# Kernel tuning notes

Measured on AMD Instinct MI355X. Metric: run time of the kernel, lower is better.

Reference implementation:

```python
import jax, jax.numpy as jnp
import numpy as np
import math

HEAD_DIM = 128
DEPTH = 12
LAMBDA_INIT = 0.8 - 0.6 * math.exp(-0.3 * DEPTH)
EPS = 1e-5


def setup_inputs() -> dict:
    key = jax.random.key(0)
    ks = jax.random.split(key, 7)
    B, S, H2, D = 2, 2048, 16, HEAD_DIM  # H2 = 2 * num_diff_heads
    q = jax.random.normal(ks[0], (B, S, H2, D), dtype=jnp.float32)
    k = jax.random.normal(ks[1], (B, S, H2, D), dtype=jnp.float32)
    v = jax.random.normal(ks[2], (B, S, H2, D), dtype=jnp.float32)
    lambda_q1 = 0.1 * jax.random.normal(ks[3], (D,), dtype=jnp.float32)
    lambda_k1 = 0.1 * jax.random.normal(ks[4], (D,), dtype=jnp.float32)
    lambda_q2 = 0.1 * jax.random.normal(ks[5], (D,), dtype=jnp.float32)
    lambda_k2 = 0.1 * jax.random.normal(ks[6], (D,), dtype=jnp.float32)
    return {"q": q, "k": k, "v": v, "lambda_q1": lambda_q1, "lambda_k1": lambda_k1,
            "lambda_q2": lambda_q2, "lambda_k2": lambda_k2}


def _attn(qh, kh, v12, scale, causal_bias):
    # qh,kh: [B,S,H,D]; v12: [B,S,H,2D] (concat of v1,v2 -> same softmax shared,
    # identical math to the two separate flash calls attnX1/attnX2 concatenated)
    scores = jnp.einsum('bshd,bthd->bhst', qh, kh) * scale + causal_bias
    p = jax.nn.softmax(scores, axis=-1)
    return jnp.einsum('bhst,bthd->bshd', p, v12)  # [B,S,H,2D]


def reference(q, k, v, lambda_q1, lambda_k1, lambda_q2, lambda_k2):
    B, S, H2, D = q.shape
    H = H2 // 2
    scale = 1.0 / math.sqrt(D)
    # split_heads: '(H two) D' -> pairs of adjacent heads
    def split(x):
        x = x.reshape(B, S, H, 2, D)
        return x[..., 0, :], x[..., 1, :]
    q1, q2 = split(q)
    k1, k2 = split(k)
    v1, v2 = split(v)
    v12 = jnp.concatenate([v1, v2], axis=-1)  # [B,S,H,2D]

    causal_bias = jnp.where(jnp.tril(jnp.ones((S, S), dtype=bool)), 0.0,
                            jnp.float32(-jnp.inf))  # [S,S]

    attn1 = _attn(q1, k1, v12, scale, causal_bias)  # = cat(attn11, attn12)
    attn2 = _attn(q2, k2, v12, scale, causal_bias)  # = cat(attn21, attn22)

    lambda_1 = jnp.exp(jnp.sum(lambda_q1 * lambda_k1))
    lambda_2 = jnp.exp(jnp.sum(lambda_q2 * lambda_k2))
    lambda_full = lambda_1 - lambda_2 + LAMBDA_INIT

    attn = attn1 - lambda_full * attn2  # [B,S,H,2D]
    # RMSNorm over last dim (2D), no affine
    attn = attn * jax.lax.rsqrt(jnp.mean(attn * attn, axis=-1, keepdims=True) + EPS)
    attn = attn * (1.0 - LAMBDA_INIT)
    # '... H (two D) -> ... (H two) D'
    return attn.reshape(B, S, H, 2, D).reshape(B, S, H2, D)
```

## Files before the change

kernel.cpp:

```cpp
#include <hip/hip_runtime.h>
#include <math.h>


#define S_LEN 2048
#define ROWSTR 2048
#define NEG_BIG (-3.0e38f)
#define QSCALE (1.44269504088896f * 0.0883883476483184f)
#define SM_SHIFT 20.0f
#define LAMBDA_INIT 0.783605766532f

typedef __attribute__((ext_vector_type(8))) short short8;
typedef __attribute__((ext_vector_type(4))) float f32x4;

__device__ __forceinline__ short f2bf(float f) {
    unsigned u = __builtin_bit_cast(unsigned, f);
    u += 0x7fffu + ((u >> 16) & 1u);
    return (short)(u >> 16);
}

__device__ __forceinline__ void async16(const short* g, short* l) {
    __builtin_amdgcn_global_load_lds(
        (const __attribute__((address_space(1))) unsigned int*)g,
        (__attribute__((address_space(3))) unsigned int*)l, 16, 0, 0);
}

__global__ __launch_bounds__(256)
void prep_kernel(const float* __restrict__ k, const float* __restrict__ v,
                 short* __restrict__ kws, short* __restrict__ vws) {
    __shared__ short sKL[8192];
    __shared__ short sT[32][260];
    const int tid = threadIdx.x;
    const int bh  = blockIdx.x >> 6;
    const int t   = blockIdx.x & 63;
    const int b   = bh >> 3;
    const int h   = bh & 7;

    {
        const int lh    = tid & 31;
        const int c     = lh >> 1;
        const int half  = lh & 1;
        const int rbase = tid >> 5;
        #pragma unroll
        for (int p = 0; p < 8; ++p) {
            const int row  = p * 8 + rbase;
            const int attn = row >> 5;
            const int key  = row & 31;
            const float* src = k + (((size_t)(b * S_LEN + t * 32 + key) * 16) + 2 * h + attn) * 128 + lh * 4;
            const float4 a = *(const float4*)src;
            short4 sv;
            sv.x = f2bf(a.x); sv.y = f2bf(a.y); sv.z = f2bf(a.z); sv.w = f2bf(a.w);
            *(short4*)(sKL + attn * 4096 + key * 128 + ((c ^ (key & 7)) << 3) + half * 4) = sv;
        }
    }

    {
        const int n0 = (tid & 63) * 4;
        const int kb = tid >> 6;
        #pragma unroll
        for (int p = 0; p < 8; ++p) {
            const int key = p * 4 + kb;
            const float* src = v + (((size_t)(b * S_LEN + t * 32 + key) * 16) + 2 * h) * 128 + n0;
            const float4 a = *(const float4*)src;
            short4 sv;
            sv.x = f2bf(a.x); sv.y = f2bf(a.y); sv.z = f2bf(a.z); sv.w = f2bf(a.w);
            *(short4*)(&sT[key][n0]) = sv;
        }
    }
    __syncthreads();

    {
        short* kdst = kws + (((size_t)(bh * 64 + t)) << 13);
        #pragma unroll
        for (int i = 0; i < 4; ++i) {
            const short8 d = *(const short8*)(sKL + i * 2048 + tid * 8);
            *(short8*)(kdst + i * 2048 + tid * 8) = d;
        }
    }

    {
        const int f = (tid >> 1) & 3;
        short vv[32];
        #pragma unroll
        for (int o = 0; o < 32; ++o)
            vv[o] = sT[(((o >> 3) ^ f) << 3) + (o & 7)][tid];
        short* vdst = vws + (((size_t)(bh * 64 + t)) << 13) + tid * 32;
        #pragma unroll
        for (int i = 0; i < 4; ++i)
            *(short8*)(vdst + i * 8) = *(short8*)&vv[i * 8];
    }
}

__global__ __launch_bounds__(256, 2)
void fda_kernel(const short* __restrict__ kws, const short* __restrict__ vws,
                const float* __restrict__ q,
                const float* __restrict__ lq1, const float* __restrict__ lk1,
                const float* __restrict__ lq2, const float* __restrict__ lk2,
                float* __restrict__ out) {
    __shared__ short sK[2][2][32][128];
    __shared__ short sV[2][256][32];
    __shared__ short sP[2][64][40];
    __shared__ float sL[2][64];
    __shared__ float sRed[2][2][32];

    const int tid  = threadIdx.x;
    const int w    = tid >> 6;
    const int lane = tid & 63;
    const int mi   = lane & 15;
    const int quad = lane >> 4;
    const int rg   = w & 1;
    const int u    = w >> 1;

    const int bid = blockIdx.x;
    const int bh  = bid & 15;
    const int g   = bid >> 4;
    const int qt  = (g < 16) ? (31 - g) : (g - 16);
    const int b   = bh >> 3;
    const int h   = bh & 7;
    const int qbase = qt * 64;
    const int nt  = 2 * qt + 2;

    const short* ktile0 = kws + (((size_t)(bh * 64)) << 13);
    const short* vtile0 = vws + (((size_t)(bh * 64)) << 13);

    {
        short* dk = &sK[0][0][0][0];
        short* dv = &sV[0][0][0];
        #pragma unroll
        for (int i = 0; i < 4; ++i) {
            const int ch = (w * 4 + i) * 512;
            async16(ktile0 + ch + lane * 8, dk + ch);
            async16(vtile0 + ch + lane * 8, dv + ch);
        }
    }

    float d1 = lq1[lane] * lk1[lane] + lq1[lane + 64] * lk1[lane + 64];
    float d2 = lq2[lane] * lk2[lane] + lq2[lane + 64] * lk2[lane + 64];
    #pragma unroll
    for (int off = 32; off; off >>= 1) {
        d1 += __shfl_xor(d1, off);
        d2 += __shfl_xor(d2, off);
    }
    const float lambda_full = expf(d1) - expf(d2) + LAMBDA_INIT;

    short8 qf[2][4];
    #pragma unroll
    for (int m = 0; m < 2; ++m) {
        const int row = qbase + rg * 32 + m * 16 + mi;
        const float* qr = q + (((size_t)(b * S_LEN + row) * 16) + 2 * h + u) * 128 + quad * 8;
        #pragma unroll
        for (int db = 0; db < 4; ++db) {
            float4 a0 = *(const float4*)(qr + db * 32);
            float4 a1 = *(const float4*)(qr + db * 32 + 4);
            short8 sv;
            sv[0]=f2bf(a0.x*QSCALE); sv[1]=f2bf(a0.y*QSCALE); sv[2]=f2bf(a0.z*QSCALE); sv[3]=f2bf(a0.w*QSCALE);
            sv[4]=f2bf(a1.x*QSCALE); sv[5]=f2bf(a1.y*QSCALE); sv[6]=f2bf(a1.z*QSCALE); sv[7]=f2bf(a1.w*QSCALE);
            qf[m][db] = sv;
        }
    }

    float l[2][4] = {{0.f,0.f,0.f,0.f},{0.f,0.f,0.f,0.f}};
    f32x4 O[2][2][8];
    #pragma unroll
    for (int a = 0; a < 2; ++a)
        #pragma unroll
        for (int m = 0; m < 2; ++m)
            #pragma unroll
            for (int nb = 0; nb < 8; ++nb)
                O[a][m][nb] = (f32x4){0.f, 0.f, 0.f, 0.f};

    const int vswz = (quad ^ ((mi >> 1) & 3)) << 3;

    for (int t = 0; t < nt; ++t) {
        __syncthreads();
        const int buf = t & 1;

        if (t + 1 < nt) {
            const short* kt = ktile0 + (((size_t)(t + 1)) << 13);
            const short* vt = vtile0 + (((size_t)(t + 1)) << 13);
            short* dk = &sK[buf ^ 1][0][0][0];
            short* dv = &sV[buf ^ 1][0][0];
            #pragma unroll
            for (int i = 0; i < 4; ++i) {
                const int ch = (w * 4 + i) * 512;
                async16(kt + ch + lane * 8, dk + ch);
                async16(vt + ch + lane * 8, dv + ch);
            }
        }

        const bool act = (t <= 2 * qt + rg);
        if (act) {
            f32x4 S[2][2];
            #pragma unroll
            for (int m = 0; m < 2; ++m)
                #pragma unroll
                for (int kh = 0; kh < 2; ++kh)
                    S[m][kh] = (f32x4){0.f, 0.f, 0.f, 0.f};
            const short* kb = &sK[buf][u][0][0];
            __builtin_amdgcn_s_setprio(1);
            #pragma unroll
            for (int db = 0; db < 4; ++db) {
                #pragma unroll
                for (int kh = 0; kh < 2; ++kh) {
                    const short8 kf = *(const short8*)(kb + (kh * 16 + mi) * 128 +
                                       ((((db << 2) + quad) ^ (mi & 7)) << 3));
                    S[0][kh] = __builtin_amdgcn_mfma_f32_16x16x32_bf16(qf[0][db], kf, S[0][kh], 0, 0, 0);
                    S[1][kh] = __builtin_amdgcn_mfma_f32_16x16x32_bf16(qf[1][db], kf, S[1][kh], 0, 0, 0);
                }
            }
            __builtin_amdgcn_s_setprio(0);
            if (t == 2 * qt + rg) {
                const int qr0 = qbase + rg * 32;
                #pragma unroll
                for (int m = 0; m < 2; ++m)
                    #pragma unroll
                    for (int kh = 0; kh < 2; ++kh)
                        #pragma unroll
                        for (int r = 0; r < 4; ++r)
                            if (t * 32 + kh * 16 + mi > qr0 + m * 16 + quad * 4 + r)
                                S[m][kh][r] = NEG_BIG;
            }
            #pragma unroll
            for (int m = 0; m < 2; ++m) {
                short* pp = &sP[u][rg * 32 + m * 16 + quad * 4][mi];
                #pragma unroll
                for (int r = 0; r < 4; ++r) {
                    const float pa = exp2f(S[m][0][r] - SM_SHIFT);
                    const float pb = exp2f(S[m][1][r] - SM_SHIFT);
                    l[m][r] += pa + pb;
                    pp[r * 40]      = f2bf(pa);
                    pp[r * 40 + 16] = f2bf(pb);
                }
            }
        }
        __syncthreads();

        if (act) {
            short8 pA[2][2];
            #pragma unroll
            for (int a = 0; a < 2; ++a)
                #pragma unroll
                for (int m = 0; m < 2; ++m)
                    pA[a][m] = *(const short8*)&sP[a][rg * 32 + m * 16 + mi][quad * 8];
            __builtin_amdgcn_s_setprio(1);
            #pragma unroll
            for (int nb = 0; nb < 8; ++nb) {
                const short8 bv = *(const short8*)&sV[buf][u * 128 + nb * 16 + mi][vswz];
                O[0][0][nb] = __builtin_amdgcn_mfma_f32_16x16x32_bf16(pA[0][0], bv, O[0][0][nb], 0, 0, 0);
                O[0][1][nb] = __builtin_amdgcn_mfma_f32_16x16x32_bf16(pA[0][1], bv, O[0][1][nb], 0, 0, 0);
                O[1][0][nb] = __builtin_amdgcn_mfma_f32_16x16x32_bf16(pA[1][0], bv, O[1][0][nb], 0, 0, 0);
                O[1][1][nb] = __builtin_amdgcn_mfma_f32_16x16x32_bf16(pA[1][1], bv, O[1][1][nb], 0, 0, 0);
            }
            __builtin_amdgcn_s_setprio(0);
        }
    }

    #pragma unroll
    for (int m = 0; m < 2; ++m)
        #pragma unroll
        for (int r = 0; r < 4; ++r) {
            float s = l[m][r];
            s += __shfl_xor(s, 1); s += __shfl_xor(s, 2);
            s += __shfl_xor(s, 4); s += __shfl_xor(s, 8);
            l[m][r] = s;
        }
    if (mi == 0) {
        #pragma unroll
        for (int m = 0; m < 2; ++m)
            #pragma unroll
            for (int r = 0; r < 4; ++r)
                sL[u][rg * 32 + m * 16 + quad * 4 + r] = l[m][r];
    }
    __syncthreads();

    float ss[2][4] = {{0.f,0.f,0.f,0.f},{0.f,0.f,0.f,0.f}};
    #pragma unroll
    for (int m = 0; m < 2; ++m)
        #pragma unroll
        for (int r = 0; r < 4; ++r) {
            const int row = rg * 32 + m * 16 + quad * 4 + r;
            const float il1 = 1.0f / sL[0][row];
            const float il2 = lambda_full / sL[1][row];
            #pragma unroll
            for (int nb = 0; nb < 8; ++nb) {
                const float c = O[0][m][nb][r] * il1 - O[1][m][nb][r] * il2;
                O[0][m][nb][r] = c;
                ss[m][r] += c * c;
            }
        }
    #pragma unroll
    for (int m = 0; m < 2; ++m)
        #pragma unroll
        for (int r = 0; r < 4; ++r) {
            float s = ss[m][r];
            s += __shfl_xor(s, 1); s += __shfl_xor(s, 2);
            s += __shfl_xor(s, 4); s += __shfl_xor(s, 8);
            ss[m][r] = s;
        }
    if (mi == 0) {
        #pragma unroll
        for (int m = 0; m < 2; ++m)
            #pragma unroll
            for (int r = 0; r < 4; ++r)
                sRed[rg][u][m * 16 + quad * 4 + r] = ss[m][r];
    }
    __syncthreads();

    #pragma unroll
    for (int m = 0; m < 2; ++m)
        #pragma unroll
        for (int r = 0; r < 4; ++r) {
            const int rl  = m * 16 + quad * 4 + r;
            const float tot = ss[m][r] + sRed[rg][u ^ 1][rl];
            const float scale = rsqrtf(tot * (1.0f / 256.0f) + 1e-5f) * (1.0f - LAMBDA_INIT);
            const int gr = qbase + rg * 32 + rl;
            float* ob = out + ((size_t)(b * S_LEN + gr)) * ROWSTR + h * 256 + u * 128 + mi;
            #pragma unroll
            for (int nb = 0; nb < 8; ++nb)
                ob[nb * 16] = O[0][m][nb][r] * scale;
        }
}

extern "C" void kernel_launch(void* const* d_in, const int* in_sizes, int n_in,
                              void* d_out, int out_size, void* d_ws, size_t ws_size,
                              hipStream_t stream) {
    (void)in_sizes; (void)n_in; (void)out_size; (void)ws_size;
    const float* q   = (const float*)d_in[0];
    const float* k   = (const float*)d_in[1];
    const float* v   = (const float*)d_in[2];
    const float* lq1 = (const float*)d_in[3];
    const float* lk1 = (const float*)d_in[4];
    const float* lq2 = (const float*)d_in[5];
    const float* lk2 = (const float*)d_in[6];
    float* out = (float*)d_out;

    short* kws = (short*)d_ws;
    short* vws = kws + (size_t)16 * 64 * 8192;

    prep_kernel<<<dim3(1024), dim3(256), 0, stream>>>(k, v, kws, vws);
    fda_kernel<<<dim3(512), dim3(256), 0, stream>>>(kws, vws, q,
                                                    lq1, lk1, lq2, lk2, out);
}
```

Before: 245.9 us.

## Software-pipeline QK and PV stages with direct K register loads

Restructures the main loop so that each iteration runs the PV product for tile t and the QK product for tile t+1. This removes one of the two barriers per iteration. K tiles are now loaded straight from global memory into registers instead of staging through LDS. V is triple-buffered with a two-tile-ahead async prefetch, and P is double-buffered. A hand-written waitcnt plus barrier replaces __syncthreads. The launch bound's minimum-blocks hint is dropped, which may raise register use and lower occupancy. The per-iteration K global loads also add latency that must be hidden.

```diff
diff --git a/kernel.cpp b/kernel.cpp
--- a/kernel.cpp
+++ b/kernel.cpp
@@ -90,15 +90,14 @@
     }
 }
 
-__global__ __launch_bounds__(256, 2)
+__global__ __launch_bounds__(256)
 void fda_kernel(const short* __restrict__ kws, const short* __restrict__ vws,
                 const float* __restrict__ q,
                 const float* __restrict__ lq1, const float* __restrict__ lk1,
                 const float* __restrict__ lq2, const float* __restrict__ lk2,
                 float* __restrict__ out) {
-    __shared__ short sK[2][2][32][128];
-    __shared__ short sV[2][256][32];
-    __shared__ short sP[2][64][40];
+    __shared__ short sV[3][256][32];
+    __shared__ short sP[2][2][64][40];
     __shared__ float sL[2][64];
     __shared__ float sRed[2][2][32];
 
@@ -118,20 +117,10 @@
     const int h   = bh & 7;
     const int qbase = qt * 64;
     const int nt  = 2 * qt + 2;
+    const int dlim = 2 * qt + rg;
 
     const short* ktile0 = kws + (((size_t)(bh * 64)) << 13);
     const short* vtile0 = vws + (((size_t)(bh * 64)) << 13);
-
-    {
-        short* dk = &sK[0][0][0][0];
-        short* dv = &sV[0][0][0];
-        #pragma unroll
-        for (int i = 0; i < 4; ++i) {
-            const int ch = (w * 4 + i) * 512;
-            async16(ktile0 + ch + lane * 8, dk + ch);
-            async16(vtile0 + ch + lane * 8, dv + ch);
-        }
-    }
 
     float d1 = lq1[lane] * lk1[lane] + lq1[lane + 64] * lk1[lane + 64];
     float d2 = lq2[lane] * lk2[lane] + lq2[lane + 64] * lk2[lane + 64];
@@ -141,6 +130,17 @@
         d2 += __shfl_xor(d2, off);
     }
     const float lambda_full = expf(d1) - expf(d2) + LAMBDA_INIT;
+
+    #pragma unroll
+    for (int i = 0; i < 4; ++i) {
+        const int ch = (w * 4 + i) * 512;
+        async16(vtile0 + ch + lane * 8, &sV[0][0][0] + ch);
+    }
+    #pragma unroll
+    for (int i = 0; i < 4; ++i) {
+        const int ch = (w * 4 + i) * 512;
+        async16(vtile0 + 8192 + ch + lane * 8, &sV[1][0][0] + ch);
+    }
 
     short8 qf[2][4];
     #pragma unroll
@@ -158,6 +158,14 @@
         }
     }
 
+    int koff[2][4];
+    #pragma unroll
+    for (int kh = 0; kh < 2; ++kh)
+        #pragma unroll
+        for (int db = 0; db < 4; ++db)
+            koff[kh][db] = u * 4096 + kh * 2048 + mi * 128 +
+                           ((((db << 2) + quad) ^ (mi & 7)) << 3);
+
     float l[2][4] = {{0.f,0.f,0.f,0.f},{0.f,0.f,0.f,0.f}};
     f32x4 O[2][2][8];
     #pragma unroll
@@ -170,45 +178,116 @@
 
     const int vswz = (quad ^ ((mi >> 1) & 3)) << 3;
 
+    {
+        short8 kf[2][4];
+        #pragma unroll
+        for (int kh = 0; kh < 2; ++kh)
+            #pragma unroll
+            for (int db = 0; db < 4; ++db)
+                kf[kh][db] = *(const short8*)(ktile0 + koff[kh][db]);
+        f32x4 S[2][2];
+        #pragma unroll
+        for (int m = 0; m < 2; ++m)
+            #pragma unroll
+            for (int kh = 0; kh < 2; ++kh)
+                S[m][kh] = (f32x4){0.f, 0.f, 0.f, 0.f};
+        __builtin_amdgcn_s_setprio(1);
+        #pragma unroll
+        for (int db = 0; db < 4; ++db)
+            #pragma unroll
+            for (int kh = 0; kh < 2; ++kh) {
+                S[0][kh] = __builtin_amdgcn_mfma_f32_16x16x32_bf16(qf[0][db], kf[kh][db], S[0][kh], 0, 0, 0);
+                S[1][kh] = __builtin_amdgcn_mfma_f32_16x16x32_bf16(qf[1][db], kf[kh][db], S[1][kh], 0, 0, 0);
+            }
+        __builtin_amdgcn_s_setprio(0);
+        if (0 == dlim) {
+            #pragma unroll
+            for (int m = 0; m < 2; ++m)
+                #pragma unroll
+                for (int kh = 0; kh < 2; ++kh)
+                    #pragma unroll
+                    for (int r = 0; r < 4; ++r)
+                        if (kh * 16 + mi > qbase + m * 16 + quad * 4 + r)
+                            S[m][kh][r] = NEG_BIG;
+        }
+        #pragma unroll
+        for (int m = 0; m < 2; ++m) {
+            short* pp = &sP[0][u][rg * 32 + m * 16 + quad * 4][mi];
+            #pragma unroll
+            for (int r = 0; r < 4; ++r) {
+                const float pa = exp2f(S[m][0][r] - SM_SHIFT);
+                const float pb = exp2f(S[m][1][r] - SM_SHIFT);
+                l[m][r] += pa + pb;
+                pp[r * 40]      = f2bf(pa);
+                pp[r * 40 + 16] = f2bf(pb);
+            }
+        }
+    }
+
     for (int t = 0; t < nt; ++t) {
-        __syncthreads();
-        const int buf = t & 1;
-
-        if (t + 1 < nt) {
+        asm volatile("s_waitcnt vmcnt(4) lgkmcnt(0)\n\ts_barrier" ::: "memory");
+        const int cur  = t % 3;
+        const int pcur = t & 1;
+        const int pnxt = (t + 1) & 1;
+        const bool act_pv = (t <= dlim);
+        const bool act_qk = (t + 1 <= dlim);
+
+        short8 kf[2][4];
+        if (act_qk) {
             const short* kt = ktile0 + (((size_t)(t + 1)) << 13);
-            const short* vt = vtile0 + (((size_t)(t + 1)) << 13);
-            short* dk = &sK[buf ^ 1][0][0][0];
-            short* dv = &sV[buf ^ 1][0][0];
+            #pragma unroll
+            for (int kh = 0; kh < 2; ++kh)
+                #pragma unroll
+                for (int db = 0; db < 4; ++db)
+                    kf[kh][db] = *(const short8*)(kt + koff[kh][db]);
+        }
+
+        if (t + 2 < nt) {
+            const short* vt = vtile0 + (((size_t)(t + 2)) << 13);
+            short* dv = &sV[(t + 2) % 3][0][0];
             #pragma unroll
             for (int i = 0; i < 4; ++i) {
                 const int ch = (w * 4 + i) * 512;
-                async16(kt + ch + lane * 8, dk + ch);
                 async16(vt + ch + lane * 8, dv + ch);
             }
         }
 
-        const bool act = (t <= 2 * qt + rg);
-        if (act) {
+        if (act_pv) {
+            short8 pA[2][2];
+            #pragma unroll
+            for (int a = 0; a < 2; ++a)
+                #pragma unroll
+                for (int m = 0; m < 2; ++m)
+                    pA[a][m] = *(const short8*)&sP[pcur][a][rg * 32 + m * 16 + mi][quad * 8];
+            __builtin_amdgcn_s_setprio(1);
+            #pragma unroll
+            for (int nb = 0; nb < 8; ++nb) {
+                const short8 bv = *(const short8*)&sV[cur][u * 128 + nb * 16 + mi][vswz];
+                O[0][0][nb] = __builtin_amdgcn_mfma_f32_16x16x32_bf16(pA[0][0], bv, O[0][0][nb], 0, 0, 0);
+                O[0][1][nb] = __builtin_amdgcn_mfma_f32_16x16x32_bf16(pA[0][1], bv, O[0][1][nb], 0, 0, 0);
+                O[1][0][nb] = __builtin_amdgcn_mfma_f32_16x16x32_bf16(pA[1][0], bv, O[1][0][nb], 0, 0, 0);
+                O[1][1][nb] = __builtin_amdgcn_mfma_f32_16x16x32_bf16(pA[1][1], bv, O[1][1][nb], 0, 0, 0);
+            }
+            __builtin_amdgcn_s_setprio(0);
+        }
+
+        if (act_qk) {
             f32x4 S[2][2];
             #pragma unroll
             for (int m = 0; m < 2; ++m)
                 #pragma unroll
                 for (int kh = 0; kh < 2; ++kh)
                     S[m][kh] = (f32x4){0.f, 0.f, 0.f, 0.f};
-            const short* kb = &sK[buf][u][0][0];
             __builtin_amdgcn_s_setprio(1);
             #pragma unroll
-            for (int db = 0; db < 4; ++db) {
+            for (int db = 0; db < 4; ++db)
                 #pragma unroll
                 for (int kh = 0; kh < 2; ++kh) {
-                    const short8 kf = *(const short8*)(kb + (kh * 16 + mi) * 128 +
-                                       ((((db << 2) + quad) ^ (mi & 7)) << 3));
-                    S[0][kh] = __builtin_amdgcn_mfma_f32_16x16x32_bf16(qf[0][db], kf, S[0][kh], 0, 0, 0);
-                    S[1][kh] = __builtin_amdgcn_mfma_f32_16x16x32_bf16(qf[1][db], kf, S[1][kh], 0, 0, 0);
+                    S[0][kh] = __builtin_amdgcn_mfma_f32_16x16x32_bf16(qf[0][db], kf[kh][db], S[0][kh], 0, 0, 0);
+                    S[1][kh] = __builtin_amdgcn_mfma_f32_16x16x32_bf16(qf[1][db], kf[kh][db], S[1][kh], 0, 0, 0);
                 }
-            }
             __builtin_amdgcn_s_setprio(0);
-            if (t == 2 * qt + rg) {
+            if (t + 1 == dlim) {
                 const int qr0 = qbase + rg * 32;
                 #pragma unroll
                 for (int m = 0; m < 2; ++m)
@@ -216,12 +295,12 @@
                     for (int kh = 0; kh < 2; ++kh)
                         #pragma unroll
                         for (int r = 0; r < 4; ++r)
-                            if (t * 32 + kh * 16 + mi > qr0 + m * 16 + quad * 4 + r)
+                            if ((t + 1) * 32 + kh * 16 + mi > qr0 + m * 16 + quad * 4 + r)
                                 S[m][kh][r] = NEG_BIG;
             }
             #pragma unroll
             for (int m = 0; m < 2; ++m) {
-                short* pp = &sP[u][rg * 32 + m * 16 + quad * 4][mi];
+                short* pp = &sP[pnxt][u][rg * 32 + m * 16 + quad * 4][mi];
                 #pragma unroll
                 for (int r = 0; r < 4; ++r) {
                     const float pa = exp2f(S[m][0][r] - SM_SHIFT);
@@ -231,26 +310,6 @@
                     pp[r * 40 + 16] = f2bf(pb);
                 }
             }
-        }
-        __syncthreads();
-
-        if (act) {
-            short8 pA[2][2];
-            #pragma unroll
-            for (int a = 0; a < 2; ++a)
-                #pragma unroll
-                for (int m = 0; m < 2; ++m)
-                    pA[a][m] = *(const short8*)&sP[a][rg * 32 + m * 16 + mi][quad * 8];
-            __builtin_amdgcn_s_setprio(1);
-            #pragma unroll
-            for (int nb = 0; nb < 8; ++nb) {
-                const short8 bv = *(const short8*)&sV[buf][u * 128 + nb * 16 + mi][vswz];
-                O[0][0][nb] = __builtin_amdgcn_mfma_f32_16x16x32_bf16(pA[0][0], bv, O[0][0][nb], 0, 0, 0);
-                O[0][1][nb] = __builtin_amdgcn_mfma_f32_16x16x32_bf16(pA[0][1], bv, O[0][1][nb], 0, 0, 0);
-                O[1][0][nb] = __builtin_amdgcn_mfma_f32_16x16x32_bf16(pA[1][0], bv, O[1][0][nb], 0, 0, 0);
-                O[1][1][nb] = __builtin_amdgcn_mfma_f32_16x16x32_bf16(pA[1][1], bv, O[1][1][nb], 0, 0, 0);
-            }
-            __builtin_amdgcn_s_setprio(0);
         }
     }
 
```

Result: slower. 320.0 us (+30.2%).

## Pack P pairs into 32-bit LDS stores and permute V key order to match

Applied to the files above, without the earlier changes.

Probabilities for keys j and j+16 are now packed into a single 32-bit LDS word, halving the number of P store instructions in the attention loop. To keep the P·V product correct, the prep kernel reorders the transposed V key layout so it matches the interleaved key order of the packed P. The prep kernel also issues all K and V global loads up front, before converting and storing them, to raise memory-level parallelism. The cost is more registers held live in prep and a tighter coupling between the P layout and the V layout.

```diff
diff --git a/kernel.cpp b/kernel.cpp
--- a/kernel.cpp
+++ b/kernel.cpp
@@ -16,6 +16,10 @@
     unsigned u = __builtin_bit_cast(unsigned, f);
     u += 0x7fffu + ((u >> 16) & 1u);
     return (short)(u >> 16);
+}
+
+__device__ __forceinline__ unsigned pack2bf(float a, float b) {
+    return (unsigned)(unsigned short)f2bf(a) | ((unsigned)(unsigned short)f2bf(b) << 16);
 }
 
 __device__ __forceinline__ void async16(const short* g, short* l) {
@@ -35,6 +39,25 @@
     const int b   = bh >> 3;
     const int h   = bh & 7;
 
+    float4 ka[8], va[8];
+    {
+        const int lh    = tid & 31;
+        const int rbase = tid >> 5;
+        #pragma unroll
+        for (int p = 0; p < 8; ++p) {
+            const int row  = p * 8 + rbase;
+            const int attn = row >> 5;
+            const int key  = row & 31;
+            ka[p] = *(const float4*)(k + (((size_t)(b * S_LEN + t * 32 + key) * 16) + 2 * h + attn) * 128 + lh * 4);
+        }
+        const int n0 = (tid & 63) * 4;
+        const int kb = tid >> 6;
+        #pragma unroll
+        for (int p = 0; p < 8; ++p) {
+            const int key = p * 4 + kb;
+            va[p] = *(const float4*)(v + (((size_t)(b * S_LEN + t * 32 + key) * 16) + 2 * h) * 128 + n0);
+        }
+    }
     {
         const int lh    = tid & 31;
         const int c     = lh >> 1;
@@ -45,24 +68,19 @@
             const int row  = p * 8 + rbase;
             const int attn = row >> 5;
             const int key  = row & 31;
-            const float* src = k + (((size_t)(b * S_LEN + t * 32 + key) * 16) + 2 * h + attn) * 128 + lh * 4;
-            const float4 a = *(const float4*)src;
             short4 sv;
-            sv.x = f2bf(a.x); sv.y = f2bf(a.y); sv.z = f2bf(a.z); sv.w = f2bf(a.w);
+            sv.x = f2bf(ka[p].x); sv.y = f2bf(ka[p].y); sv.z = f2bf(ka[p].z); sv.w = f2bf(ka[p].w);
             *(short4*)(sKL + attn * 4096 + key * 128 + ((c ^ (key & 7)) << 3) + half * 4) = sv;
         }
     }
-
     {
         const int n0 = (tid & 63) * 4;
         const int kb = tid >> 6;
         #pragma unroll
         for (int p = 0; p < 8; ++p) {
             const int key = p * 4 + kb;
-            const float* src = v + (((size_t)(b * S_LEN + t * 32 + key) * 16) + 2 * h) * 128 + n0;
-            const float4 a = *(const float4*)src;
             short4 sv;
-            sv.x = f2bf(a.x); sv.y = f2bf(a.y); sv.z = f2bf(a.z); sv.w = f2bf(a.w);
+            sv.x = f2bf(va[p].x); sv.y = f2bf(va[p].y); sv.z = f2bf(va[p].z); sv.w = f2bf(va[p].w);
             *(short4*)(&sT[key][n0]) = sv;
         }
     }
@@ -81,8 +99,10 @@
         const int f = (tid >> 1) & 3;
         short vv[32];
         #pragma unroll
-        for (int o = 0; o < 32; ++o)
-            vv[o] = sT[(((o >> 3) ^ f) << 3) + (o & 7)][tid];
+        for (int p = 0; p < 4; ++p)
+            #pragma unroll
+            for (int s = 0; s < 8; ++s)
+                vv[p * 8 + s] = sT[((p ^ f) << 2) + (s >> 1) + ((s & 1) << 4)][tid];
         short* vdst = vws + (((size_t)(bh * 64 + t)) << 13) + tid * 32;
         #pragma unroll
         for (int i = 0; i < 4; ++i)
@@ -98,7 +118,7 @@
                 float* __restrict__ out) {
     __shared__ short sK[2][2][32][128];
     __shared__ short sV[2][256][32];
-    __shared__ short sP[2][64][40];
+    __shared__ unsigned sP2[2][64][20];
     __shared__ float sL[2][64];
     __shared__ float sRed[2][2][32];
 
@@ -221,14 +241,13 @@
             }
             #pragma unroll
             for (int m = 0; m < 2; ++m) {
-                short* pp = &sP[u][rg * 32 + m * 16 + quad * 4][mi];
+                unsigned* pp = &sP2[u][rg * 32 + m * 16 + quad * 4][mi];
                 #pragma unroll
                 for (int r = 0; r < 4; ++r) {
                     const float pa = exp2f(S[m][0][r] - SM_SHIFT);
                     const float pb = exp2f(S[m][1][r] - SM_SHIFT);
                     l[m][r] += pa + pb;
-                    pp[r * 40]      = f2bf(pa);
-                    pp[r * 40 + 16] = f2bf(pb);
+                    pp[r * 20] = pack2bf(pa, pb);
                 }
             }
         }
@@ -240,7 +259,7 @@
             for (int a = 0; a < 2; ++a)
                 #pragma unroll
                 for (int m = 0; m < 2; ++m)
-                    pA[a][m] = *(const short8*)&sP[a][rg * 32 + m * 16 + mi][quad * 8];
+                    pA[a][m] = *(const short8*)&sP2[a][rg * 32 + m * 16 + mi][quad * 4];
             __builtin_amdgcn_s_setprio(1);
             #pragma unroll
             for (int nb = 0; nb < 8; ++nb) {
```

New measurement: 246.6 us. No clear change (+0.3%).
